# Optimization experiments

Hardware: AMD Instinct MI355X
Metric: run time of the kernel (lower is better)

## Reference

```python
import jax, jax.numpy as jnp
import numpy as np

# Sizes
NC, NT, NP = 100000, 300000, 50000   # customers, transactions, products
F, DIMC = 8, 16                      # columns per table, per-column embed dim
D = F * DIMC                         # 128 = proj_dim (lazy SAGEConv in-channels)
L, R = 2, 4                          # gnn layers, relation types
OUT = 10                             # out_channels
EM, EI = 300000, 600000              # edges: customer-makes-transaction, product-in-transaction


def setup_inputs() -> dict:
    key = jax.random.key(0)
    ks = jax.random.split(key, 14)
    s = 0.05
    return {
        "x_c": jax.random.normal(ks[0], (NC, F), jnp.float32),
        "x_t": jax.random.normal(ks[1], (NT, F), jnp.float32),
        "x_p": jax.random.normal(ks[2], (NP, F), jnp.float32),
        # per-table per-column numeric embedders: scalar -> DIMC (w*x + b)
        "W_col": jax.random.normal(ks[3], (3, F, DIMC), jnp.float32) * s,
        "b_col": jax.random.normal(ks[4], (3, F, DIMC), jnp.float32) * s,
        # SAGEConv weights per layer per relation: lin_l (neighbor) and lin_r (root)
        "Wn": jax.random.normal(ks[5], (L, R, D, D), jnp.float32) * s,
        "Wr": jax.random.normal(ks[6], (L, R, D, D), jnp.float32) * s,
        "b_lin": jax.random.normal(ks[7], (L, R, D), jnp.float32) * s,
        "W_out": jax.random.normal(ks[8], (D, OUT), jnp.float32) * s,
        "b_out": jax.random.normal(ks[9], (OUT,), jnp.float32) * s,
        "e_makes_src": jax.random.randint(ks[10], (EM,), 0, NC, jnp.int32),
        "e_makes_dst": jax.random.randint(ks[11], (EM,), 0, NT, jnp.int32),
        "e_in_src": jax.random.randint(ks[12], (EI,), 0, NP, jnp.int32),
        "e_in_dst": jax.random.randint(ks[13], (EI,), 0, NT, jnp.int32),
    }


def _embed(x, W, b):
    # x: [N, F]; W,b: [F, DIMC] -> [N, F*DIMC] (concat of per-column embeddings)
    n = x.shape[0]
    return (x[:, :, None] * W[None] + b[None]).reshape(n, -1)


def _sage(x_src, x_dst, src, dst, Wn, Wr, b, n_dst):
    # SAGEConv(mean): out = mean_neigh(x_src) @ Wn + b + x_dst @ Wr
    msg = jax.ops.segment_sum(x_src[src], dst, num_segments=n_dst)
    cnt = jax.ops.segment_sum(jnp.ones(src.shape[0], x_src.dtype), dst, num_segments=n_dst)
    mean = msg / jnp.maximum(cnt, 1.0)[:, None]  # isolated nodes -> 0 message
    return mean @ Wn + x_dst @ Wr + b


def reference(x_c, x_t, x_p, W_col, b_col, Wn, Wr, b_lin, W_out, b_out,
              e_makes_src, e_makes_dst, e_in_src, e_in_dst):
    h_c = _embed(x_c, W_col[0], b_col[0])
    h_t = _embed(x_t, W_col[1], b_col[1])
    h_p = _embed(x_p, W_col[2], b_col[2])
    for l in range(L):
        # R0: customer -makes-> transaction
        o_t0 = _sage(h_c, h_t, e_makes_src, e_makes_dst, Wn[l, 0], Wr[l, 0], b_lin[l, 0], NT)
        # R1: transaction -rev_makes-> customer
        o_c = _sage(h_t, h_c, e_makes_dst, e_makes_src, Wn[l, 1], Wr[l, 1], b_lin[l, 1], NC)
        # R2: product -in-> transaction
        o_t2 = _sage(h_p, h_t, e_in_src, e_in_dst, Wn[l, 2], Wr[l, 2], b_lin[l, 2], NT)
        # R3: transaction -rev_in-> product
        o_p = _sage(h_t, h_p, e_in_dst, e_in_src, Wn[l, 3], Wr[l, 3], b_lin[l, 3], NP)
        # HeteroConv(aggr='mean'): mean over relations targeting each dst type
        h_c, h_t, h_p = o_c, 0.5 * (o_t0 + o_t2), o_p
    logits = h_t @ W_out + b_out  # target_table = 'transaction'
    return jax.nn.softmax(logits, axis=1)
```

## Files before the change

kernel.cpp:

```cpp
#include <hip/hip_runtime.h>

#define NCV 100000
#define NTV 300000
#define NPV 50000
#define DD 128
#define OUTC 10
#define EMV 300000
#define EIV 600000
#define YST 16
#define NHEADS (NCV + NPV + 2 * NTV)
#define HIB ((NHEADS + 255) / 256)
#define PTB ((3 * 1280 * 64) / 256)
#define NEB ((EIV + 255) / 256)
#define BDB ((450 * 64 + 255) / 256)
#define GYB ((NCV + NPV + 255) / 256)

__device__ __forceinline__ float i2f(int v) { return __int_as_float(v); }

__global__ __launch_bounds__(256) void init_prepT(
    int* __restrict__ heads,
    const float* __restrict__ Wn10, const float* __restrict__ Wn12,
    const float* __restrict__ Wr10, const float* __restrict__ Wr12,
    const float* __restrict__ Wout, float* __restrict__ T) {
  int b = blockIdx.x;
  int tid = threadIdx.x;
  if (b < HIB) {
    int i = b * 256 + tid;
    if (i < NHEADS) heads[i] = -1;
    return;
  }
  int gw = ((b - HIB) * 256 + tid) >> 6;
  int lane = tid & 63;
  if (gw >= 3 * 1280) return;
  int mat = gw / 1280, r = gw % 1280, n = r / 10, o = r % 10;
  float s = 0.f;
  #pragma unroll
  for (int mi = 0; mi < 2; ++mi) {
    int m = lane + mi * 64;
    float w;
    if (mat == 0) w = Wn10[n * 128 + m];
    else if (mat == 1) w = Wn12[n * 128 + m];
    else w = 0.5f * (Wr10[n * 128 + m] + Wr12[n * 128 + m]);
    s += w * Wout[m * 10 + o];
  }
  #pragma unroll
  for (int d = 32; d; d >>= 1) s += __shfl_xor(s, d);
  if (lane == 0) T[gw] = s;
}

__global__ __launch_bounds__(256) void build_prepB(
    const int* __restrict__ ems, const int* __restrict__ emd,
    const int* __restrict__ eis, const int* __restrict__ eid,
    const float* __restrict__ xt,
    int* __restrict__ head_c, int* __restrict__ head_p,
    int* __restrict__ heads_t,
    int4* __restrict__ cnm, int4* __restrict__ cni,
    int2* __restrict__ tn_m, int2* __restrict__ tn_i,
    const float* __restrict__ Wn, const float* __restrict__ Wr,
    const float* __restrict__ Wcol, const float* __restrict__ bcol,
    const float* __restrict__ b_lin, const float* __restrict__ Wout,
    const float* __restrict__ bout,
    const float* __restrict__ T, float* __restrict__ B) {
  int b = blockIdx.x;
  int tid = threadIdx.x;
  if (b < NEB) {
    int e = b * 256 + tid;
    if (e < EMV) {
      int c = ems[e], t = emd[e];
      int cn = atomicExch(&head_c[c], e);
      int tn = atomicExch(&heads_t[2 * t], e);
      const int4* xr = (const int4*)(xt + (size_t)t * 8);
      int4 x0 = xr[0], x1 = xr[1];
      size_t bb = 4 * (size_t)e;
      cnm[bb]     = make_int4(cn, x0.x, x0.y, x0.z);
      cnm[bb + 1] = make_int4(x0.w, x1.x, x1.y, x1.z);
      cnm[bb + 2] = make_int4(x1.w, 0, 0, 0);
      tn_m[e] = make_int2(tn, c);
    }
    if (e < EIV) {
      int p = eis[e], t = eid[e];
      int pn = atomicExch(&head_p[p], e);
      int tn = atomicExch(&heads_t[2 * t + 1], e);
      const int4* xr = (const int4*)(xt + (size_t)t * 8);
      int4 x0 = xr[0], x1 = xr[1];
      size_t bb = 4 * (size_t)e;
      cni[bb]     = make_int4(pn, x0.x, x0.y, x0.z);
      cni[bb + 1] = make_int4(x0.w, x1.x, x1.y, x1.z);
      cni[bb + 2] = make_int4(x1.w, 0, 0, 0);
      tn_i[e] = make_int2(tn, p);
    }
    return;
  }

  int gw = ((b - NEB) * 256 + tid) >> 6;
  int lane = tid & 63;
  if (gw >= 450) return;
  int r = gw / 10, o = gw % 10;
  int n0 = lane, n1 = lane + 64;

  const float* Wn00 = Wn;               const float* Wn01 = Wn + 16384;
  const float* Wn02 = Wn + 2 * 16384;   const float* Wn03 = Wn + 3 * 16384;
  const float* Wr00 = Wr;               const float* Wr01 = Wr + 16384;
  const float* Wr02 = Wr + 2 * 16384;   const float* Wr03 = Wr + 3 * 16384;
  const float* WcC = Wcol, *WcT = Wcol + 128, *WcP = Wcol + 256;
  const float* bC = bcol, *bT = bcol + 128, *bP = bcol + 256;
  const float* b00 = b_lin, *b01 = b_lin + 128, *b02 = b_lin + 256, *b03 = b_lin + 384;
  const float* b10 = b_lin + 512, *b12 = b_lin + 768;
  const float* T1 = T, *T2 = T + 1280, *T3 = T + 2560;

  float a1_0 = 0.f, a1_1 = 0.f;
  float a2_0 = 0.f, a2_1 = 0.f;
  float a3_0 = 0.f, a3_1 = 0.f;
  float extra = 0.f;

  if (r < 8) {
    for (int j = 0; j < 16; ++j) {
      float c = WcT[r * 16 + j]; int k = r * 16 + j;
      a1_0 += c * Wn01[k * 128 + n0]; a1_1 += c * Wn01[k * 128 + n1];
    }
  } else if (r < 16) {
    int j0 = r - 8;
    for (int j = 0; j < 16; ++j) {
      float c = WcC[j0 * 16 + j]; int k = j0 * 16 + j;
      a1_0 += c * Wr01[k * 128 + n0]; a1_1 += c * Wr01[k * 128 + n1];
      a3_0 += c * Wn00[k * 128 + n0]; a3_1 += c * Wn00[k * 128 + n1];
    }
  } else if (r == 16) {
    for (int k = 0; k < 128; ++k) {
      float c = bT[k];
      a1_0 += c * Wn01[k * 128 + n0]; a1_1 += c * Wn01[k * 128 + n1];
    }
  } else if (r < 25) {
    int j0 = r - 17;
    for (int j = 0; j < 16; ++j) {
      float c = WcT[j0 * 16 + j]; int k = j0 * 16 + j;
      a2_0 += c * Wn03[k * 128 + n0]; a2_1 += c * Wn03[k * 128 + n1];
    }
  } else if (r < 33) {
    int j0 = r - 25;
    for (int j = 0; j < 16; ++j) {
      float c = WcP[j0 * 16 + j]; int k = j0 * 16 + j;
      a2_0 += c * Wr03[k * 128 + n0]; a2_1 += c * Wr03[k * 128 + n1];
      a3_0 += c * Wn02[k * 128 + n0]; a3_1 += c * Wn02[k * 128 + n1];
    }
  } else if (r == 33) {
    for (int k = 0; k < 128; ++k) {
      float c = bT[k];
      a2_0 += c * Wn03[k * 128 + n0]; a2_1 += c * Wn03[k * 128 + n1];
    }
  } else if (r < 42) {
    int j0 = r - 34;
    for (int j = 0; j < 16; ++j) {
      float c = WcT[j0 * 16 + j]; int k = j0 * 16 + j;
      a3_0 += c * (Wr00[k * 128 + n0] + Wr02[k * 128 + n0]);
      a3_1 += c * (Wr00[k * 128 + n1] + Wr02[k * 128 + n1]);
    }
  } else if (r == 42) {
    for (int k = 0; k < 128; ++k) {
      float c = bC[k];
      a1_0 += c * Wr01[k * 128 + n0]; a1_1 += c * Wr01[k * 128 + n1];
      a3_0 += c * Wn00[k * 128 + n0]; a3_1 += c * Wn00[k * 128 + n1];
    }
    a1_0 += b01[n0]; a1_1 += b01[n1];
  } else if (r == 43) {
    for (int k = 0; k < 128; ++k) {
      float c = bP[k];
      a2_0 += c * Wr03[k * 128 + n0]; a2_1 += c * Wr03[k * 128 + n1];
      a3_0 += c * Wn02[k * 128 + n0]; a3_1 += c * Wn02[k * 128 + n1];
    }
    a2_0 += b03[n0]; a2_1 += b03[n1];
  } else {
    for (int k = 0; k < 128; ++k) {
      float c = bT[k];
      a3_0 += c * (Wr00[k * 128 + n0] + Wr02[k * 128 + n0]);
      a3_1 += c * (Wr00[k * 128 + n1] + Wr02[k * 128 + n1]);
    }
    a3_0 += b00[n0] + b02[n0]; a3_1 += b00[n1] + b02[n1];
    extra = (b10[n0] + b12[n0]) * Wout[n0 * 10 + o] +
            (b10[n1] + b12[n1]) * Wout[n1 * 10 + o];
  }

  float s = a1_0 * T1[n0 * 10 + o] + a1_1 * T1[n1 * 10 + o] +
            a2_0 * T2[n0 * 10 + o] + a2_1 * T2[n1 * 10 + o] +
            a3_0 * T3[n0 * 10 + o] + a3_1 * T3[n1 * 10 + o] + extra;
  #pragma unroll
  for (int d = 32; d; d >>= 1) s += __shfl_xor(s, d);
  if (lane == 0) {
    float v = 0.5f * s;
    if (r == 44) v += bout[o];
    B[gw] = v;
  }
}

__global__ __launch_bounds__(256) void gather_y(
    const int* __restrict__ head_c, const int* __restrict__ head_p,
    const int4* __restrict__ cnm, const int4* __restrict__ cni,
    const float* __restrict__ xc, const float* __restrict__ xp,
    const float* __restrict__ B,
    float* __restrict__ y_c, float* __restrict__ y_p) {
  __shared__ float sB[340];
  int tid = threadIdx.x;
  for (int i = tid; i < 340; i += 256) sB[i] = B[i];
  __syncthreads();
  int i = blockIdx.x * 256 + tid;
  if (i >= NCV + NPV) return;
  bool isC = i < NCV;
  int idx = isC ? i : i - NCV;
  const int4* cn = isC ? cnm : cni;
  int e = isC ? head_c[idx] : head_p[idx];

  float acc[8] = {0.f, 0.f, 0.f, 0.f, 0.f, 0.f, 0.f, 0.f};
  float cnt = 0.f;
  while (e >= 0) {
    size_t bb = 4 * (size_t)e;
    int4 w0 = cn[bb];
    int4 w1 = cn[bb + 1];
    int4 w2 = cn[bb + 2];
    acc[0] += i2f(w0.y); acc[1] += i2f(w0.z); acc[2] += i2f(w0.w);
    acc[3] += i2f(w1.x); acc[4] += i2f(w1.y); acc[5] += i2f(w1.z); acc[6] += i2f(w1.w);
    acc[7] += i2f(w2.x);
    cnt += 1.f;
    e = w0.x;
  }

  const float* xo = (isC ? xc : xp) + (size_t)idx * 8;
  const float* Bs = sB + (isC ? 0 : 170);
  float gg = cnt > 0.f ? 1.f : 0.f;
  float inv = gg / fmaxf(cnt, 1.f);
  float lg[OUTC];
  #pragma unroll
  for (int o = 0; o < OUTC; ++o) lg[o] = gg * Bs[16 * 10 + o];
  #pragma unroll
  for (int r = 0; r < 8; ++r) {
    float zb = acc[r] * inv;
    float zo = xo[r];
    #pragma unroll
    for (int o = 0; o < OUTC; ++o)
      lg[o] += zb * Bs[r * 10 + o] + zo * Bs[(8 + r) * 10 + o];
  }
  float4* yv = (float4*)((isC ? y_c : y_p) + (size_t)idx * YST);
  yv[0] = make_float4(lg[0], lg[1], lg[2], lg[3]);
  yv[1] = make_float4(lg[4], lg[5], lg[6], lg[7]);
  yv[2] = make_float4(lg[8], lg[9], 0.f, 0.f);
  yv[3] = make_float4(0.f, 0.f, 0.f, 0.f);
}

__global__ __launch_bounds__(256) void gather_t(
    const float* __restrict__ y_c, const float* __restrict__ y_p,
    const float* __restrict__ xt,
    const int* __restrict__ heads_t,
    const int2* __restrict__ tn_m, const int2* __restrict__ tn_i,
    const float* __restrict__ B, float* __restrict__ out) {
  __shared__ float sB[110];
  int tid = threadIdx.x;
  for (int i = tid; i < 110; i += 256) sB[i] = B[340 + i];
  __syncthreads();
  int t = blockIdx.x * 256 + tid;
  if (t >= NTV) return;

  int2 ht = ((const int2*)heads_t)[t];
  int e1 = ht.x, e2 = ht.y;

  float sc[OUTC] = {0.f, 0.f, 0.f, 0.f, 0.f, 0.f, 0.f, 0.f, 0.f, 0.f};
  float sp[OUTC] = {0.f, 0.f, 0.f, 0.f, 0.f, 0.f, 0.f, 0.f, 0.f, 0.f};
  float dc = 0.f, dp = 0.f;
  while (e1 >= 0 || e2 >= 0) {
    if (e1 >= 0) {
      int2 v = tn_m[e1];
      const float* yr = y_c + (size_t)v.y * YST;
      float4 u = *(const float4*)yr;
      float4 w = *(const float4*)(yr + 4);
      float2 z = *(const float2*)(yr + 8);
      sc[0] += u.x; sc[1] += u.y; sc[2] += u.z; sc[3] += u.w;
      sc[4] += w.x; sc[5] += w.y; sc[6] += w.z; sc[7] += w.w;
      sc[8] += z.x; sc[9] += z.y;
      dc += 1.f;
      e1 = v.x;
    }
    if (e2 >= 0) {
      int2 v = tn_i[e2];
      const float* yr = y_p + (size_t)v.y * YST;
      float4 u = *(const float4*)yr;
      float4 w = *(const float4*)(yr + 4);
      float2 z = *(const float2*)(yr + 8);
      sp[0] += u.x; sp[1] += u.y; sp[2] += u.z; sp[3] += u.w;
      sp[4] += w.x; sp[5] += w.y; sp[6] += w.z; sp[7] += w.w;
      sp[8] += z.x; sp[9] += z.y;
      dp += 1.f;
      e2 = v.x;
    }
  }

  float Gc = dc > 0.f ? 1.f : 0.f, Gp = dp > 0.f ? 1.f : 0.f;
  float ivc = 1.f / fmaxf(dc, 1.f), ivp = 1.f / fmaxf(dp, 1.f);

  const float4* xp4 = (const float4*)(xt + (size_t)t * 8);
  float4 xa = xp4[0], xb = xp4[1];
  float xv[8] = {xa.x, xa.y, xa.z, xa.w, xb.x, xb.y, xb.z, xb.w};

  float lg[OUTC];
  #pragma unroll
  for (int o = 0; o < OUTC; ++o)
    lg[o] = sc[o] * ivc + sp[o] * ivp +
            Gc * sB[80 + o] + Gp * sB[90 + o] + sB[100 + o];
  #pragma unroll
  for (int r = 0; r < 8; ++r) {
    float xr = xv[r];
    #pragma unroll
    for (int o = 0; o < OUTC; ++o) lg[o] += xr * sB[r * 10 + o];
  }

  float m = lg[0];
  #pragma unroll
  for (int o = 1; o < OUTC; ++o) m = fmaxf(m, lg[o]);
  float s = 0.f;
  #pragma unroll
  for (int o = 0; o < OUTC; ++o) { lg[o] = __expf(lg[o] - m); s += lg[o]; }
  float invs = 1.0f / s;
  float* op = &out[(size_t)t * OUTC];
  #pragma unroll
  for (int o = 0; o < 5; ++o) {
    float2 p2; p2.x = lg[2 * o] * invs; p2.y = lg[2 * o + 1] * invs;
    *(float2*)&op[2 * o] = p2;
  }
}

extern "C" void kernel_launch(void* const* d_in, const int* in_sizes, int n_in,
                              void* d_out, int out_size, void* d_ws, size_t ws_size,
                              hipStream_t stream) {
  const float* x_c   = (const float*)d_in[0];
  const float* x_t   = (const float*)d_in[1];
  const float* x_p   = (const float*)d_in[2];
  const float* W_col = (const float*)d_in[3];
  const float* b_col = (const float*)d_in[4];
  const float* Wn    = (const float*)d_in[5];
  const float* Wr    = (const float*)d_in[6];
  const float* b_lin = (const float*)d_in[7];
  const float* W_out = (const float*)d_in[8];
  const float* b_out = (const float*)d_in[9];
  const int* e_m_src = (const int*)d_in[10];
  const int* e_m_dst = (const int*)d_in[11];
  const int* e_i_src = (const int*)d_in[12];
  const int* e_i_dst = (const int*)d_in[13];
  float* out = (float*)d_out;

  size_t cursor = 0;
  char* base = (char*)d_ws;
  auto alloc = [&](size_t bytes) {
    void* p = base + cursor;
    cursor += (bytes + 255) & ~(size_t)255;
    return p;
  };
  int* heads   = (int*)alloc((size_t)NHEADS * 4);
  int* head_c  = heads;
  int* head_p  = heads + NCV;
  int* heads_t = heads + NCV + NPV;
  int4* cnm = (int4*)alloc((size_t)EMV * 64);
  int4* cni = (int4*)alloc((size_t)EIV * 64);
  int2* tn_m = (int2*)alloc((size_t)EMV * 8);
  int2* tn_i = (int2*)alloc((size_t)EIV * 8);
  float* y_c = (float*)alloc((size_t)NCV * YST * 4);
  float* y_p = (float*)alloc((size_t)NPV * YST * 4);
  float* T   = (float*)alloc(3 * 1280 * 4);
  float* B   = (float*)alloc(450 * 4);

  const float* Wn10 = Wn + 4 * (size_t)DD * DD;
  const float* Wn12 = Wn + 6 * (size_t)DD * DD;
  const float* Wr10 = Wr + 4 * (size_t)DD * DD;
  const float* Wr12 = Wr + 6 * (size_t)DD * DD;

  init_prepT<<<HIB + PTB, 256, 0, stream>>>(
      heads, Wn10, Wn12, Wr10, Wr12, W_out, T);

  build_prepB<<<NEB + BDB, 256, 0, stream>>>(
      e_m_src, e_m_dst, e_i_src, e_i_dst, x_t,
      head_c, head_p, heads_t, cnm, cni, tn_m, tn_i,
      Wn, Wr, W_col, b_col, b_lin, W_out, b_out, T, B);

  gather_y<<<GYB, 256, 0, stream>>>(
      head_c, head_p, cnm, cni, x_c, x_p, B, y_c, y_p);

  gather_t<<<(NTV + 255) / 256, 256, 0, stream>>>(
      y_c, y_p, x_t, heads_t, tn_m, tn_i, B, out);
}
```

Before: 224.0 us.

## Fold T-matrix computation into B-coefficient kernel and decouple graph build

Removes the separate T intermediate: each B warp now recomputes the needed W·Wout columns inline, so the B coefficient computation moves from the graph-build kernel into the init kernel alongside head initialization. The graph-build kernel becomes a pure edge-linking kernel. This removes the cross-kernel dependency on T and shortens the build kernel. The cost is redundant weight-matrix reads and extra dot products in each of the 450 warps.

After: 253.4 us. 1.13x slower.

```diff
diff --git a/kernel.cpp b/kernel.cpp
--- a/kernel.cpp
+++ b/kernel.cpp
@@ -10,18 +10,18 @@
 #define YST 16
 #define NHEADS (NCV + NPV + 2 * NTV)
 #define HIB ((NHEADS + 255) / 256)
-#define PTB ((3 * 1280 * 64) / 256)
+#define BFB ((450 * 64 + 255) / 256)
 #define NEB ((EIV + 255) / 256)
-#define BDB ((450 * 64 + 255) / 256)
 #define GYB ((NCV + NPV + 255) / 256)
 
 __device__ __forceinline__ float i2f(int v) { return __int_as_float(v); }
 
-__global__ __launch_bounds__(256) void init_prepT(
+__global__ __launch_bounds__(256) void init_B(
     int* __restrict__ heads,
-    const float* __restrict__ Wn10, const float* __restrict__ Wn12,
-    const float* __restrict__ Wr10, const float* __restrict__ Wr12,
-    const float* __restrict__ Wout, float* __restrict__ T) {
+    const float* __restrict__ Wn, const float* __restrict__ Wr,
+    const float* __restrict__ Wcol, const float* __restrict__ bcol,
+    const float* __restrict__ b_lin, const float* __restrict__ Wout,
+    const float* __restrict__ bout, float* __restrict__ B) {
   int b = blockIdx.x;
   int tid = threadIdx.x;
   if (b < HIB) {
@@ -31,164 +31,161 @@
   }
   int gw = ((b - HIB) * 256 + tid) >> 6;
   int lane = tid & 63;
-  if (gw >= 3 * 1280) return;
-  int mat = gw / 1280, r = gw % 1280, n = r / 10, o = r % 10;
-  float s = 0.f;
-  #pragma unroll
-  for (int mi = 0; mi < 2; ++mi) {
-    int m = lane + mi * 64;
-    float w;
-    if (mat == 0) w = Wn10[n * 128 + m];
-    else if (mat == 1) w = Wn12[n * 128 + m];
-    else w = 0.5f * (Wr10[n * 128 + m] + Wr12[n * 128 + m]);
-    s += w * Wout[m * 10 + o];
-  }
+  if (gw >= 450) return;
+  int r = gw / 10, o = gw % 10;
+  int n0 = lane, n1 = lane + 64;
+
+  const float* Wn00 = Wn;               const float* Wn01 = Wn + 16384;
+  const float* Wn02 = Wn + 2 * 16384;   const float* Wn03 = Wn + 3 * 16384;
+  const float* Wn10 = Wn + 4 * 16384;   const float* Wn12 = Wn + 6 * 16384;
+  const float* Wr00 = Wr;               const float* Wr01 = Wr + 16384;
+  const float* Wr02 = Wr + 2 * 16384;   const float* Wr03 = Wr + 3 * 16384;
+  const float* Wr10 = Wr + 4 * 16384;   const float* Wr12 = Wr + 6 * 16384;
+  const float* WcC = Wcol, *WcT = Wcol + 128, *WcP = Wcol + 256;
+  const float* bC = bcol, *bT = bcol + 128, *bP = bcol + 256;
+  const float* b00 = b_lin, *b01 = b_lin + 128, *b02 = b_lin + 256, *b03 = b_lin + 384;
+  const float* b10 = b_lin + 512, *b12 = b_lin + 768;
+
+  float a1_0 = 0.f, a1_1 = 0.f;
+  float a2_0 = 0.f, a2_1 = 0.f;
+  float a3_0 = 0.f, a3_1 = 0.f;
+  float extra = 0.f;
+
+  if (r < 8) {
+    for (int j = 0; j < 16; ++j) {
+      float c = WcT[r * 16 + j]; int k = r * 16 + j;
+      a1_0 += c * Wn01[k * 128 + n0]; a1_1 += c * Wn01[k * 128 + n1];
+    }
+  } else if (r < 16) {
+    int j0 = r - 8;
+    for (int j = 0; j < 16; ++j) {
+      float c = WcC[j0 * 16 + j]; int k = j0 * 16 + j;
+      a1_0 += c * Wr01[k * 128 + n0]; a1_1 += c * Wr01[k * 128 + n1];
+      a3_0 += c * Wn00[k * 128 + n0]; a3_1 += c * Wn00[k * 128 + n1];
+    }
+  } else if (r == 16) {
+    for (int k = 0; k < 128; ++k) {
+      float c = bT[k];
+      a1_0 += c * Wn01[k * 128 + n0]; a1_1 += c * Wn01[k * 128 + n1];
+    }
+  } else if (r < 25) {
+    int j0 = r - 17;
+    for (int j = 0; j < 16; ++j) {
+      float c = WcT[j0 * 16 + j]; int k = j0 * 16 + j;
+      a2_0 += c * Wn03[k * 128 + n0]; a2_1 += c * Wn03[k * 128 + n1];
+    }
+  } else if (r < 33) {
+    int j0 = r - 25;
+    for (int j = 0; j < 16; ++j) {
+      float c = WcP[j0 * 16 + j]; int k = j0 * 16 + j;
+      a2_0 += c * Wr03[k * 128 + n0]; a2_1 += c * Wr03[k * 128 + n1];
+      a3_0 += c * Wn02[k * 128 + n0]; a3_1 += c * Wn02[k * 128 + n1];
+    }
+  } else if (r == 33) {
+    for (int k = 0; k < 128; ++k) {
+      float c = bT[k];
+      a2_0 += c * Wn03[k * 128 + n0]; a2_1 += c * Wn03[k * 128 + n1];
+    }
+  } else if (r < 42) {
+    int j0 = r - 34;
+    for (int j = 0; j < 16; ++j) {
+      float c = WcT[j0 * 16 + j]; int k = j0 * 16 + j;
+      a3_0 += c * (Wr00[k * 128 + n0] + Wr02[k * 128 + n0]);
+      a3_1 += c * (Wr00[k * 128 + n1] + Wr02[k * 128 + n1]);
+    }
+  } else if (r == 42) {
+    for (int k = 0; k < 128; ++k) {
+      float c = bC[k];
+      a1_0 += c * Wr01[k * 128 + n0]; a1_1 += c * Wr01[k * 128 + n1];
+      a3_0 += c * Wn00[k * 128 + n0]; a3_1 += c * Wn00[k * 128 + n1];
+    }
+    a1_0 += b01[n0]; a1_1 += b01[n1];
+  } else if (r == 43) {
+    for (int k = 0; k < 128; ++k) {
+      float c = bP[k];
+      a2_0 += c * Wr03[k * 128 + n0]; a2_1 += c * Wr03[k * 128 + n1];
+      a3_0 += c * Wn02[k * 128 + n0]; a3_1 += c * Wn02[k * 128 + n1];
+    }
+    a2_0 += b03[n0]; a2_1 += b03[n1];
+  } else {
+    for (int k = 0; k < 128; ++k) {
+      float c = bT[k];
+      a3_0 += c * (Wr00[k * 128 + n0] + Wr02[k * 128 + n0]);
+      a3_1 += c * (Wr00[k * 128 + n1] + Wr02[k * 128 + n1]);
+    }
+    a3_0 += b00[n0] + b02[n0]; a3_1 += b00[n1] + b02[n1];
+    extra = (b10[n0] + b12[n0]) * Wout[n0 * 10 + o] +
+            (b10[n1] + b12[n1]) * Wout[n1 * 10 + o];
+  }
+
+  bool use1 = (r < 17) || (r == 42);
+  bool use2 = (r >= 17 && r < 34) || (r == 43);
+  bool use3 = (r >= 8 && r < 16) || (r >= 25 && r < 33) || (r >= 34);
+  float t1_0 = 0.f, t1_1 = 0.f, t2_0 = 0.f, t2_1 = 0.f, t3_0 = 0.f, t3_1 = 0.f;
+  if (use1) {
+    for (int m = 0; m < 128; ++m) {
+      float w = Wout[m * 10 + o];
+      t1_0 += Wn10[n0 * 128 + m] * w; t1_1 += Wn10[n1 * 128 + m] * w;
+    }
+  }
+  if (use2) {
+    for (int m = 0; m < 128; ++m) {
+      float w = Wout[m * 10 + o];
+      t2_0 += Wn12[n0 * 128 + m] * w; t2_1 += Wn12[n1 * 128 + m] * w;
+    }
+  }
+  if (use3) {
+    for (int m = 0; m < 128; ++m) {
+      float w = Wout[m * 10 + o];
+      t3_0 += 0.5f * (Wr10[n0 * 128 + m] + Wr12[n0 * 128 + m]) * w;
+      t3_1 += 0.5f * (Wr10[n1 * 128 + m] + Wr12[n1 * 128 + m]) * w;
+    }
+  }
+
+  float s = a1_0 * t1_0 + a1_1 * t1_1 +
+            a2_0 * t2_0 + a2_1 * t2_1 +
+            a3_0 * t3_0 + a3_1 * t3_1 + extra;
   #pragma unroll
   for (int d = 32; d; d >>= 1) s += __shfl_xor(s, d);
-  if (lane == 0) T[gw] = s;
-}
-
-__global__ __launch_bounds__(256) void build_prepB(
+  if (lane == 0) {
+    float v = 0.5f * s;
+    if (r == 44) v += bout[o];
+    B[gw] = v;
+  }
+}
+
+__global__ __launch_bounds__(256) void build_graph(
     const int* __restrict__ ems, const int* __restrict__ emd,
     const int* __restrict__ eis, const int* __restrict__ eid,
     const float* __restrict__ xt,
     int* __restrict__ head_c, int* __restrict__ head_p,
     int* __restrict__ heads_t,
     int4* __restrict__ cnm, int4* __restrict__ cni,
-    int2* __restrict__ tn_m, int2* __restrict__ tn_i,
-    const float* __restrict__ Wn, const float* __restrict__ Wr,
-    const float* __restrict__ Wcol, const float* __restrict__ bcol,
-    const float* __restrict__ b_lin, const float* __restrict__ Wout,
-    const float* __restrict__ bout,
-    const float* __restrict__ T, float* __restrict__ B) {
-  int b = blockIdx.x;
-  int tid = threadIdx.x;
-  if (b < NEB) {
-    int e = b * 256 + tid;
-    if (e < EMV) {
-      int c = ems[e], t = emd[e];
-      int cn = atomicExch(&head_c[c], e);
-      int tn = atomicExch(&heads_t[2 * t], e);
-      const int4* xr = (const int4*)(xt + (size_t)t * 8);
-      int4 x0 = xr[0], x1 = xr[1];
-      size_t bb = 4 * (size_t)e;
-      cnm[bb]     = make_int4(cn, x0.x, x0.y, x0.z);
-      cnm[bb + 1] = make_int4(x0.w, x1.x, x1.y, x1.z);
-      cnm[bb + 2] = make_int4(x1.w, 0, 0, 0);
-      tn_m[e] = make_int2(tn, c);
-    }
-    if (e < EIV) {
-      int p = eis[e], t = eid[e];
-      int pn = atomicExch(&head_p[p], e);
-      int tn = atomicExch(&heads_t[2 * t + 1], e);
-      const int4* xr = (const int4*)(xt + (size_t)t * 8);
-      int4 x0 = xr[0], x1 = xr[1];
-      size_t bb = 4 * (size_t)e;
-      cni[bb]     = make_int4(pn, x0.x, x0.y, x0.z);
-      cni[bb + 1] = make_int4(x0.w, x1.x, x1.y, x1.z);
-      cni[bb + 2] = make_int4(x1.w, 0, 0, 0);
-      tn_i[e] = make_int2(tn, p);
-    }
-    return;
-  }
-
-  int gw = ((b - NEB) * 256 + tid) >> 6;
-  int lane = tid & 63;
-  if (gw >= 450) return;
-  int r = gw / 10, o = gw % 10;
-  int n0 = lane, n1 = lane + 64;
-
-  const float* Wn00 = Wn;               const float* Wn01 = Wn + 16384;
-  const float* Wn02 = Wn + 2 * 16384;   const float* Wn03 = Wn + 3 * 16384;
-  const float* Wr00 = Wr;               const float* Wr01 = Wr + 16384;
-  const float* Wr02 = Wr + 2 * 16384;   const float* Wr03 = Wr + 3 * 16384;
-  const float* WcC = Wcol, *WcT = Wcol + 128, *WcP = Wcol + 256;
-  const float* bC = bcol, *bT = bcol + 128, *bP = bcol + 256;
-  const float* b00 = b_lin, *b01 = b_lin + 128, *b02 = b_lin + 256, *b03 = b_lin + 384;
-  const float* b10 = b_lin + 512, *b12 = b_lin + 768;
-  const float* T1 = T, *T2 = T + 1280, *T3 = T + 2560;
-
-  float a1_0 = 0.f, a1_1 = 0.f;
-  float a2_0 = 0.f, a2_1 = 0.f;
-  float a3_0 = 0.f, a3_1 = 0.f;
-  float extra = 0.f;
-
-  if (r < 8) {
-    for (int j = 0; j < 16; ++j) {
-      float c = WcT[r * 16 + j]; int k = r * 16 + j;
-      a1_0 += c * Wn01[k * 128 + n0]; a1_1 += c * Wn01[k * 128 + n1];
-    }
-  } else if (r < 16) {
-    int j0 = r - 8;
-    for (int j = 0; j < 16; ++j) {
-      float c = WcC[j0 * 16 + j]; int k = j0 * 16 + j;
-      a1_0 += c * Wr01[k * 128 + n0]; a1_1 += c * Wr01[k * 128 + n1];
-      a3_0 += c * Wn00[k * 128 + n0]; a3_1 += c * Wn00[k * 128 + n1];
-    }
-  } else if (r == 16) {
-    for (int k = 0; k < 128; ++k) {
-      float c = bT[k];
-      a1_0 += c * Wn01[k * 128 + n0]; a1_1 += c * Wn01[k * 128 + n1];
-    }
-  } else if (r < 25) {
-    int j0 = r - 17;
-    for (int j = 0; j < 16; ++j) {
-      float c = WcT[j0 * 16 + j]; int k = j0 * 16 + j;
-      a2_0 += c * Wn03[k * 128 + n0]; a2_1 += c * Wn03[k * 128 + n1];
-    }
-  } else if (r < 33) {
-    int j0 = r - 25;
-    for (int j = 0; j < 16; ++j) {
-      float c = WcP[j0 * 16 + j]; int k = j0 * 16 + j;
-      a2_0 += c * Wr03[k * 128 + n0]; a2_1 += c * Wr03[k * 128 + n1];
-      a3_0 += c * Wn02[k * 128 + n0]; a3_1 += c * Wn02[k * 128 + n1];
-    }
-  } else if (r == 33) {
-    for (int k = 0; k < 128; ++k) {
-      float c = bT[k];
-      a2_0 += c * Wn03[k * 128 + n0]; a2_1 += c * Wn03[k * 128 + n1];
-    }
-  } else if (r < 42) {
-    int j0 = r - 34;
-    for (int j = 0; j < 16; ++j) {
-      float c = WcT[j0 * 16 + j]; int k = j0 * 16 + j;
-      a3_0 += c * (Wr00[k * 128 + n0] + Wr02[k * 128 + n0]);
-      a3_1 += c * (Wr00[k * 128 + n1] + Wr02[k * 128 + n1]);
-    }
-  } else if (r == 42) {
-    for (int k = 0; k < 128; ++k) {
-      float c = bC[k];
-      a1_0 += c * Wr01[k * 128 + n0]; a1_1 += c * Wr01[k * 128 + n1];
-      a3_0 += c * Wn00[k * 128 + n0]; a3_1 += c * Wn00[k * 128 + n1];
-    }
-    a1_0 += b01[n0]; a1_1 += b01[n1];
-  } else if (r == 43) {
-    for (int k = 0; k < 128; ++k) {
-      float c = bP[k];
-      a2_0 += c * Wr03[k * 128 + n0]; a2_1 += c * Wr03[k * 128 + n1];
-      a3_0 += c * Wn02[k * 128 + n0]; a3_1 += c * Wn02[k * 128 + n1];
-    }
-    a2_0 += b03[n0]; a2_1 += b03[n1];
-  } else {
-    for (int k = 0; k < 128; ++k) {
-      float c = bT[k];
-      a3_0 += c * (Wr00[k * 128 + n0] + Wr02[k * 128 + n0]);
-      a3_1 += c * (Wr00[k * 128 + n1] + Wr02[k * 128 + n1]);
-    }
-    a3_0 += b00[n0] + b02[n0]; a3_1 += b00[n1] + b02[n1];
-    extra = (b10[n0] + b12[n0]) * Wout[n0 * 10 + o] +
-            (b10[n1] + b12[n1]) * Wout[n1 * 10 + o];
-  }
-
-  float s = a1_0 * T1[n0 * 10 + o] + a1_1 * T1[n1 * 10 + o] +
-            a2_0 * T2[n0 * 10 + o] + a2_1 * T2[n1 * 10 + o] +
-            a3_0 * T3[n0 * 10 + o] + a3_1 * T3[n1 * 10 + o] + extra;
-  #pragma unroll
-  for (int d = 32; d; d >>= 1) s += __shfl_xor(s, d);
-  if (lane == 0) {
-    float v = 0.5f * s;
-    if (r == 44) v += bout[o];
-    B[gw] = v;
+    int2* __restrict__ tn_m, int2* __restrict__ tn_i) {
+  int e = blockIdx.x * 256 + threadIdx.x;
+  if (e < EMV) {
+    int c = ems[e], t = emd[e];
+    int cn = atomicExch(&head_c[c], e);
+    int tn = atomicExch(&heads_t[2 * t], e);
+    const int4* xr = (const int4*)(xt + (size_t)t * 8);
+    int4 x0 = xr[0], x1 = xr[1];
+    size_t bb = 4 * (size_t)e;
+    cnm[bb]     = make_int4(cn, x0.x, x0.y, x0.z);
+    cnm[bb + 1] = make_int4(x0.w, x1.x, x1.y, x1.z);
+    cnm[bb + 2] = make_int4(x1.w, 0, 0, 0);
+    tn_m[e] = make_int2(tn, c);
+  }
+  if (e < EIV) {
+    int p = eis[e], t = eid[e];
+    int pn = atomicExch(&head_p[p], e);
+    int tn = atomicExch(&heads_t[2 * t + 1], e);
+    const int4* xr = (const int4*)(xt + (size_t)t * 8);
+    int4 x0 = xr[0], x1 = xr[1];
+    size_t bb = 4 * (size_t)e;
+    cni[bb]     = make_int4(pn, x0.x, x0.y, x0.z);
+    cni[bb + 1] = make_int4(x0.w, x1.x, x1.y, x1.z);
+    cni[bb + 2] = make_int4(x1.w, 0, 0, 0);
+    tn_i[e] = make_int2(tn, p);
   }
 }
 
@@ -361,21 +358,14 @@
   int2* tn_i = (int2*)alloc((size_t)EIV * 8);
   float* y_c = (float*)alloc((size_t)NCV * YST * 4);
   float* y_p = (float*)alloc((size_t)NPV * YST * 4);
-  float* T   = (float*)alloc(3 * 1280 * 4);
   float* B   = (float*)alloc(450 * 4);
 
-  const float* Wn10 = Wn + 4 * (size_t)DD * DD;
-  const float* Wn12 = Wn + 6 * (size_t)DD * DD;
-  const float* Wr10 = Wr + 4 * (size_t)DD * DD;
-  const float* Wr12 = Wr + 6 * (size_t)DD * DD;
-
-  init_prepT<<<HIB + PTB, 256, 0, stream>>>(
-      heads, Wn10, Wn12, Wr10, Wr12, W_out, T);
-
-  build_prepB<<<NEB + BDB, 256, 0, stream>>>(
+  init_B<<<HIB + BFB, 256, 0, stream>>>(
+      heads, Wn, Wr, W_col, b_col, b_lin, W_out, b_out, B);
+
+  build_graph<<<NEB, 256, 0, stream>>>(
       e_m_src, e_m_dst, e_i_src, e_i_dst, x_t,
-      head_c, head_p, heads_t, cnm, cni, tn_m, tn_i,
-      Wn, Wr, W_col, b_col, b_lin, W_out, b_out, T, B);
+      head_c, head_p, heads_t, cnm, cni, tn_m, tn_i);
 
   gather_y<<<GYB, 256, 0, stream>>>(
       head_c, head_p, cnm, cni, x_c, x_p, B, y_c, y_p);
```
